# Kernel tuning notes

Hardware: AMD Instinct MI355X
Metric: run time of the kernel (lower is better)

The kernel has to match this reference:

```python
import jax, jax.numpy as jnp
import numpy as np

B, E, H, N = 16, 1024, 16, 2048
Eh = E // H   # head dim = 64
BH = B * H    # 256


def setup_inputs() -> dict:
    key = jax.random.key(0)
    ks = jax.random.split(key, 12)
    query = jax.random.normal(ks[0], (B, E), jnp.float32)
    key_in = jax.random.normal(ks[1], (B, E), jnp.float32)
    value = jax.random.normal(ks[2], (B, E), jnp.float32)
    # State as it would look in steady state: a_sum ~ O(N) positive,
    # q_mem stores already-scaled queries (small), k/v unit-ish scale.
    a_sum_mem = float(N) * (0.9 + 0.2 * jax.random.uniform(ks[3], (BH, N - 1), jnp.float32))
    av_mem = (0.1 * float(N)) * jax.random.normal(ks[4], (BH, N - 1, Eh), jnp.float32)
    q_mem = 0.06 * jax.random.normal(ks[5], (BH, N, Eh), jnp.float32)
    k_t_mem = 0.5 * jax.random.normal(ks[6], (BH, Eh, N), jnp.float32)
    v_mem = 0.5 * jax.random.normal(ks[7], (BH, N, Eh), jnp.float32)
    in_proj_weight = 0.02 * jax.random.normal(ks[8], (3 * E, E), jnp.float32)
    in_proj_bias = jnp.zeros((3 * E,), jnp.float32)
    out_proj_weight = 0.02 * jax.random.normal(ks[9], (E, E), jnp.float32)
    out_proj_bias = jnp.zeros((E,), jnp.float32)
    return dict(query=query, key=key_in, value=value,
                a_sum_mem=a_sum_mem, av_mem=av_mem, q_mem=q_mem,
                k_t_mem=k_t_mem, v_mem=v_mem,
                in_proj_weight=in_proj_weight, in_proj_bias=in_proj_bias,
                out_proj_weight=out_proj_weight, out_proj_bias=out_proj_bias)


def _sdpa_step(a_sum_mem, av_mem, q_mem, k_t_mem, v_mem, q_step, k_step, v_step):
    # Faithful port of _scaled_dot_product_attention_step.
    q_step = q_step / jnp.sqrt(jnp.float32(Eh))          # (BH, Eh)
    q_old = q_mem[:, 0]                                   # (BH, Eh)
    k_old = k_t_mem[:, :, 0]                              # (BH, Eh)
    q_sel = jnp.stack((q_old, q_step), axis=1)            # (BH, 2, Eh)
    k_sel = jnp.stack((k_old, k_step), axis=2)            # (BH, Eh, 2)
    a_tb = jnp.exp(jnp.einsum('bte,bes->bts', q_sel, k_t_mem[:, :, 1:]))  # (BH, 2, N-1)
    a_lr = jnp.exp(jnp.einsum('bne,bet->bnt', q_mem[:, 1:, :], k_sel))    # (BH, N-1, 2)
    a_br = jnp.exp(jnp.sum(q_step * k_step, axis=1))      # (BH,)
    a_sum = jnp.concatenate(
        [a_sum_mem + a_lr[:, :, 1] - a_lr[:, :, 0],
         (a_tb[:, 1].sum(axis=1) + a_br)[:, None]], axis=1)               # (BH, N)
    av_top = (av_mem
              - a_lr[:, :, 0, None] * v_mem[:, 0][:, None, :]
              + a_lr[:, :, 1, None] * v_step[:, None, :])                 # (BH, N-1, Eh)
    av_bot = jnp.einsum('bs,bse->be', a_tb[:, 1], v_mem[:, 1:]) + a_br[:, None] * v_step
    av = jnp.concatenate([av_top, av_bot[:, None, :]], axis=1)            # (BH, N, Eh)
    out = av / a_sum[..., None]
    new_state = (a_sum[:, 1:], av[:, 1:],
                 jnp.concatenate([q_mem[:, 1:], q_step[:, None, :]], axis=1),
                 jnp.concatenate([k_t_mem[:, :, 1:], k_step[:, :, None]], axis=2),
                 jnp.concatenate([v_mem[:, 1:], v_step[:, None, :]], axis=1))
    return out, new_state


def reference(query, key, value, a_sum_mem, av_mem, q_mem, k_t_mem, v_mem,
              in_proj_weight, in_proj_bias, out_proj_weight, out_proj_bias):
    # Packed in-projection (q/k/v chunks of the packed weight).
    w_q, w_k, w_v = jnp.split(in_proj_weight, 3, axis=0)
    b_q, b_k, b_v = jnp.split(in_proj_bias, 3)
    q = (query @ w_q.T + b_q).reshape(BH, Eh)   # head split: (B, H*Eh) -> (B*H, Eh)
    k = (key @ w_k.T + b_k).reshape(BH, Eh)
    v = (value @ w_v.T + b_v).reshape(BH, Eh)
    attn, new_state = _sdpa_step(a_sum_mem, av_mem, q_mem, k_t_mem, v_mem, q, k, v)
    # (BH, N, Eh) -> (N, BH, Eh) -> (N, B, E), then output projection.
    attn = attn.transpose(1, 0, 2).reshape(N, B, E)
    out = attn @ out_proj_weight.T + out_proj_bias    # (N, B, E)
    return (out,) + new_state
```

## Files before the change

kernel.cpp:

```cpp
#include <hip/hip_runtime.h>
#include <hip/hip_bf16.h>

constexpr int kB  = 16;
constexpr int kE  = 1024;
constexpr int kH  = 16;
constexpr int kN  = 2048;
constexpr int kEh = 64;
constexpr int kBH = 256;
constexpr int kM  = kN * kB;

typedef __bf16 bf16x8 __attribute__((ext_vector_type(8)));
typedef float  f32x4  __attribute__((ext_vector_type(4)));
typedef unsigned short u16x4 __attribute__((ext_vector_type(4)));

static __device__ __forceinline__ unsigned short bf16_bits(float f) {
  union { __hip_bfloat16 h; unsigned short u; } cv;
  cv.h = __float2bfloat16(f);
  return cv.u;
}

static __device__ __forceinline__ f32x4 nt_load4(const float* p) {
  return __builtin_nontemporal_load(reinterpret_cast<const f32x4*>(p));
}
static __device__ __forceinline__ void nt_store4(float* p, f32x4 v) {
  __builtin_nontemporal_store(v, reinterpret_cast<f32x4*>(p));
}

__global__ __launch_bounds__(256) void prep_kernel(
    const float* __restrict__ query, const float* __restrict__ key_in,
    const float* __restrict__ value, const float* __restrict__ W,
    const float* __restrict__ bias,
    float* __restrict__ q_step, float* __restrict__ k_step,
    float* __restrict__ v_step,
    const float* __restrict__ wo, __hip_bfloat16* __restrict__ wo_bf) {
  __shared__ float red[4][16];
  int bid = blockIdx.x;
  int tid = threadIdx.x;
  if (bid >= 3072) {
    int i4 = ((bid - 3072) * 256 + tid) * 4;
    f32x4 w4 = nt_load4(wo + i4);
    u16x4 o;
    o[0] = bf16_bits(w4[0]); o[1] = bf16_bits(w4[1]);
    o[2] = bf16_bits(w4[2]); o[3] = bf16_bits(w4[3]);
    *reinterpret_cast<u16x4*>(reinterpret_cast<unsigned short*>(wo_bf) + i4) = o;
    return;
  }
  int j   = bid;
  int mat = j >> 10;
  int col = j & 1023;
  const float* in = (mat == 0) ? query : ((mat == 1) ? key_in : value);
  const float* wrow = W + (size_t)j * kE;

  float4 w4 = reinterpret_cast<const float4*>(wrow)[tid];
  float part[16];
#pragma unroll
  for (int r = 0; r < 16; ++r) {
    float4 in4 = reinterpret_cast<const float4*>(in + (size_t)r * kE)[tid];
    part[r] = w4.x * in4.x + w4.y * in4.y + w4.z * in4.z + w4.w * in4.w;
  }
#pragma unroll
  for (int r = 0; r < 16; ++r) {
    float v = part[r];
    for (int off = 32; off > 0; off >>= 1) v += __shfl_down(v, off, 64);
    part[r] = v;
  }
  int wave = tid >> 6;
  int lane = tid & 63;
  if (lane == 0) {
#pragma unroll
    for (int r = 0; r < 16; ++r) red[wave][r] = part[r];
  }
  __syncthreads();
  if (tid < 16) {
    int r = tid;
    float v = red[0][r] + red[1][r] + red[2][r] + red[3][r] + bias[j];
    int h = col >> 6, eh = col & 63;
    int bh = r * kH + h;
    if (mat == 0)      q_step[bh * kEh + eh] = v * 0.125f;
    else if (mat == 1) k_step[bh * kEh + eh] = v;
    else               v_step[bh * kEh + eh] = v;
  }
}

__global__ __launch_bounds__(256) void stream_kernel(
    const float* __restrict__ q_mem, const float* __restrict__ av_mem,
    const float* __restrict__ a_sum_mem, const float* __restrict__ k_t_mem,
    const float* __restrict__ v_mem, const float* __restrict__ q_step,
    const float* __restrict__ k_step, const float* __restrict__ v_step,
    float* __restrict__ q_out, float* __restrict__ av_out,
    float* __restrict__ a_sum_out, float* __restrict__ k_t_out,
    float* __restrict__ v_out, float* __restrict__ top_sum,
    float* __restrict__ av_last, __hip_bfloat16* __restrict__ attn) {
  __shared__ float qs[64];
  __shared__ float tbuf[1024];
  __shared__ f32x4 redv[4][16];
  __shared__ float redt[4];

  int bid = blockIdx.x;
  int tid = threadIdx.x;
  int wave = tid >> 6, lane = tid & 63;

  if (bid < 8192) {
    int b = bid >> 5;
    int chunk = bid & 31;
    int g = lane >> 4, c = lane & 15;
    int b_ = b >> 4, h = b & 15;

    f32x4 kst  = *reinterpret_cast<const f32x4*>(k_step + (size_t)b * kEh + c * 4);
    f32x4 vst  = *reinterpret_cast<const f32x4*>(v_step + (size_t)b * kEh + c * 4);
    f32x4 vold = *reinterpret_cast<const f32x4*>(v_mem + (size_t)b * kN * kEh + c * 4);
    const float* kt0 = k_t_mem + (size_t)b * kEh * kN;
    f32x4 kold;
    kold[0] = kt0[(size_t)(4 * c + 0) * kN];
    kold[1] = kt0[(size_t)(4 * c + 1) * kN];
    kold[2] = kt0[(size_t)(4 * c + 2) * kN];
    kold[3] = kt0[(size_t)(4 * c + 3) * kN];

    unsigned short* attn_u = reinterpret_cast<unsigned short*>(attn);

    int jb = chunk * 64 + wave * 16;
#pragma unroll
    for (int it = 0; it < 4; ++it) {
      int j = jb + it * 4 + g;
      bool valid = (j <= kN - 2);
      int jc = valid ? j : (kN - 2);

      f32x4 q4 = nt_load4(q_mem + ((size_t)b * kN + (jc + 1)) * kEh + c * 4);
      float p0 = q4[0] * kold[0] + q4[1] * kold[1] + q4[2] * kold[2] + q4[3] * kold[3];
      float p1 = q4[0] * kst[0]  + q4[1] * kst[1]  + q4[2] * kst[2]  + q4[3] * kst[3];
#pragma unroll
      for (int off = 1; off < 16; off <<= 1) {
        p0 += __shfl_xor(p0, off, 64);
        p1 += __shfl_xor(p1, off, 64);
      }
      float a0 = __expf(p0);
      float a1 = __expf(p1);
      float asum = a_sum_mem[(size_t)b * (kN - 1) + jc] + a1 - a0;
      f32x4 av4 = nt_load4(av_mem + ((size_t)b * (kN - 1) + jc) * kEh + c * 4);
      f32x4 avv;
      avv[0] = av4[0] - a0 * vold[0] + a1 * vst[0];
      avv[1] = av4[1] - a0 * vold[1] + a1 * vst[1];
      avv[2] = av4[2] - a0 * vold[2] + a1 * vst[2];
      avv[3] = av4[3] - a0 * vold[3] + a1 * vst[3];

      if (valid) {
        nt_store4(q_out + ((size_t)b * kN + jc) * kEh + c * 4, q4);
        float inv = 1.0f / asum;
        u16x4 pk;
        pk[0] = bf16_bits(avv[0] * inv);
        pk[1] = bf16_bits(avv[1] * inv);
        pk[2] = bf16_bits(avv[2] * inv);
        pk[3] = bf16_bits(avv[3] * inv);
        *reinterpret_cast<u16x4*>(
            attn_u + ((size_t)jc * kB + b_) * kE + h * kEh + c * 4) = pk;
        if (j >= 1) {
          nt_store4(av_out + ((size_t)b * (kN - 1) + (jc - 1)) * kEh + c * 4, avv);
          if (c == 0) a_sum_out[(size_t)b * (kN - 1) + (jc - 1)] = asum;
        }
      }
    }
    return;
  }

  int id2 = bid - 8192;
  int b = id2 >> 1, chunk = id2 & 1;

  if (tid < 64) qs[tid] = q_step[b * kEh + tid];
  __syncthreads();

  int c4 = chunk * 1024 + tid * 4;
  bool last = (c4 + 4 >= kN);
  const float* src = k_t_mem + (size_t)b * kEh * kN;
  float* dst = k_t_out + (size_t)b * kEh * kN;

  f32x4 dot = {0.f, 0.f, 0.f, 0.f};
#pragma unroll 4
  for (int e = 0; e < 64; ++e) {
    f32x4 a = nt_load4(src + (size_t)e * kN + c4);
    float s3 = last ? 0.f
                    : __builtin_nontemporal_load(src + (size_t)e * kN + c4 + 4);
    f32x4 sh;
    sh[0] = a[1]; sh[1] = a[2]; sh[2] = a[3]; sh[3] = s3;
    nt_store4(dst + (size_t)e * kN + c4, sh);
    float q = qs[e];
    dot[0] += q * sh[0];
    dot[1] += q * sh[1];
    dot[2] += q * sh[2];
    dot[3] += q * sh[3];
  }
  float tx = __expf(dot[0]);
  float ty = __expf(dot[1]);
  float tz = __expf(dot[2]);
  float tw = last ? 0.f : __expf(dot[3]);

  tbuf[tid * 4 + 0] = tx;
  tbuf[tid * 4 + 1] = ty;
  tbuf[tid * 4 + 2] = tz;
  tbuf[tid * 4 + 3] = tw;

  float s = tx + ty + tz + tw;
  for (int off = 32; off > 0; off >>= 1) s += __shfl_xor(s, off, 64);
  if (lane == 0) redt[wave] = s;
  __syncthreads();
  if (tid == 0)
    atomicAdd(&top_sum[b], redt[0] + redt[1] + redt[2] + redt[3]);

  int g = lane >> 4, c = lane & 15;
  const float* vsrc = v_mem + (size_t)b * kN * kEh;
  float* vdst = v_out + (size_t)b * kN * kEh;

  f32x4 acc = {0.f, 0.f, 0.f, 0.f};
  int sbase = chunk * 1024 + wave * 256;
#pragma unroll 4
  for (int it = 0; it < 64; ++it) {
    int s4 = sbase + it * 4 + g;
    bool valid = (s4 <= kN - 2);
    int sc = valid ? s4 : (kN - 2);
    float t = valid ? tbuf[s4 - chunk * 1024] : 0.f;
    f32x4 vv = nt_load4(vsrc + (size_t)(sc + 1) * kEh + c * 4);
    acc[0] += t * vv[0];
    acc[1] += t * vv[1];
    acc[2] += t * vv[2];
    acc[3] += t * vv[3];
    if (valid) nt_store4(vdst + (size_t)sc * kEh + c * 4, vv);
  }
#pragma unroll
  for (int off = 16; off <= 32; off <<= 1) {
    acc[0] += __shfl_xor(acc[0], off, 64);
    acc[1] += __shfl_xor(acc[1], off, 64);
    acc[2] += __shfl_xor(acc[2], off, 64);
    acc[3] += __shfl_xor(acc[3], off, 64);
  }
  if (g == 0) redv[wave][c] = acc;
  __syncthreads();
  if (tid < 16) {
    f32x4 a0 = redv[0][tid];
    f32x4 a1 = redv[1][tid];
    f32x4 a2 = redv[2][tid];
    f32x4 a3 = redv[3][tid];
    float* dstl = av_last + (size_t)b * kEh + tid * 4;
    atomicAdd(dstl + 0, a0[0] + a1[0] + a2[0] + a3[0]);
    atomicAdd(dstl + 1, a0[1] + a1[1] + a2[1] + a3[1]);
    atomicAdd(dstl + 2, a0[2] + a1[2] + a2[2] + a3[2]);
    atomicAdd(dstl + 3, a0[3] + a1[3] + a2[3] + a3[3]);
  }
}

__global__ __launch_bounds__(64) void final_kernel(
    const float* __restrict__ q_step, const float* __restrict__ k_step,
    const float* __restrict__ v_step, const float* __restrict__ top_sum,
    const float* __restrict__ av_last_in, float* __restrict__ q_out,
    float* __restrict__ k_t_out, float* __restrict__ v_out,
    float* __restrict__ a_sum_out, float* __restrict__ av_out,
    __hip_bfloat16* __restrict__ attn) {
  int b = blockIdx.x;
  int lane = threadIdx.x;
  int b_ = b >> 4, h = b & 15;
  float qs = q_step[b * kEh + lane];
  float ks = k_step[b * kEh + lane];
  float vs = v_step[b * kEh + lane];
  float p = qs * ks;
  for (int off = 32; off > 0; off >>= 1) p += __shfl_xor(p, off, 64);
  float abr = __expf(p);
  float asum = top_sum[b] + abr;
  float avl = av_last_in[b * kEh + lane] + abr * vs;
  attn[((size_t)(kN - 1) * kB + b_) * kE + h * kEh + lane] =
      __float2bfloat16(avl / asum);
  if (lane == 0) a_sum_out[(size_t)b * (kN - 1) + (kN - 2)] = asum;
  av_out[((size_t)b * (kN - 1) + (kN - 2)) * kEh + lane] = avl;
  q_out[((size_t)b * kN + (kN - 1)) * kEh + lane] = qs;
  k_t_out[(size_t)b * kEh * kN + (size_t)lane * kN + (kN - 1)] = ks;
  v_out[((size_t)b * kN + (kN - 1)) * kEh + lane] = vs;
}

#define BM 128
#define BN 128
#define BK 64

__global__ __launch_bounds__(256) void gemm_kernel(
    const __bf16* __restrict__ A, const __bf16* __restrict__ Bw,
    const float* __restrict__ bias, float* __restrict__ C,
    int M, int Ncols, int K) {
  __shared__ __bf16 lA[BM * BK];
  __shared__ __bf16 lB[BN * BK];
  int tid = threadIdx.x;
  int m0 = blockIdx.x * BM;
  int n0 = blockIdx.y * BN;
  int wave = tid >> 6;
  int lane = tid & 63;
  int wm = (wave & 1) * 64;
  int wn = (wave >> 1) * 64;

  f32x4 zero = {0.f, 0.f, 0.f, 0.f};
  f32x4 acc[4][4];
#pragma unroll
  for (int i = 0; i < 4; ++i)
#pragma unroll
    for (int j = 0; j < 4; ++j) acc[i][j] = zero;

  int quad = lane >> 4;
  int mrow = lane & 15;

  for (int k0 = 0; k0 < K; k0 += BK) {
#pragma unroll
    for (int r = 0; r < 4; ++r) {
      int off = r * 4096 + tid * 16;
      int row = off >> 7;
      int col8 = (off >> 4) & 7;
      const __bf16* ga = A + ((size_t)(m0 + row) * K + k0 + col8 * 8);
      const __bf16* gb = Bw + ((size_t)(n0 + row) * K + k0 + col8 * 8);
      __builtin_amdgcn_global_load_lds(
          (const __attribute__((address_space(1))) void*)ga,
          (__attribute__((address_space(3))) void*)((char*)lA + off), 16, 0, 0);
      __builtin_amdgcn_global_load_lds(
          (const __attribute__((address_space(1))) void*)gb,
          (__attribute__((address_space(3))) void*)((char*)lB + off), 16, 0, 0);
    }
    __syncthreads();

#pragma unroll
    for (int kk = 0; kk < 2; ++kk) {
      bf16x8 af[4], bfr[4];
#pragma unroll
      for (int i = 0; i < 4; ++i) {
        af[i]  = *(const bf16x8*)(&lA[(wm + i * 16 + mrow) * BK + kk * 32 + quad * 8]);
        bfr[i] = *(const bf16x8*)(&lB[(wn + i * 16 + mrow) * BK + kk * 32 + quad * 8]);
      }
#pragma unroll
      for (int i = 0; i < 4; ++i)
#pragma unroll
        for (int j = 0; j < 4; ++j)
          acc[i][j] = __builtin_amdgcn_mfma_f32_16x16x32_bf16(
              af[i], bfr[j], acc[i][j], 0, 0, 0);
    }
    __syncthreads();
  }

  int colq = lane & 15;
  int rowq = lane >> 4;
#pragma unroll
  for (int i = 0; i < 4; ++i) {
#pragma unroll
    for (int j = 0; j < 4; ++j) {
      int col = n0 + wn + j * 16 + colq;
      float bv = bias[col];
      size_t base = (size_t)(m0 + wm + i * 16 + rowq * 4) * Ncols + col;
#pragma unroll
      for (int r = 0; r < 4; ++r) {
        __builtin_nontemporal_store(acc[i][j][r] + bv,
                                    &C[base + (size_t)r * Ncols]);
      }
    }
  }
}

extern "C" void kernel_launch(void* const* d_in, const int* in_sizes, int n_in,
                              void* d_out, int out_size, void* d_ws,
                              size_t ws_size, hipStream_t stream) {
  const float* query          = (const float*)d_in[0];
  const float* key_in         = (const float*)d_in[1];
  const float* value          = (const float*)d_in[2];
  const float* a_sum_mem      = (const float*)d_in[3];
  const float* av_mem         = (const float*)d_in[4];
  const float* q_mem          = (const float*)d_in[5];
  const float* k_t_mem        = (const float*)d_in[6];
  const float* v_mem          = (const float*)d_in[7];
  const float* in_proj_weight = (const float*)d_in[8];
  const float* in_proj_bias   = (const float*)d_in[9];
  const float* out_proj_weight= (const float*)d_in[10];
  const float* out_proj_bias  = (const float*)d_in[11];

  float* out       = (float*)d_out;
  float* a_sum_out = out + (size_t)kN * kB * kE;
  float* av_out    = a_sum_out + (size_t)kBH * (kN - 1);
  float* q_out     = av_out + (size_t)kBH * (kN - 1) * kEh;
  float* k_t_out   = q_out + (size_t)kBH * kN * kEh;
  float* v_out     = k_t_out + (size_t)kBH * kEh * kN;

  char* ws = (char*)d_ws;
  float* q_step  = (float*)ws;
  float* k_step  = q_step + 16384;
  float* v_step  = k_step + 16384;
  float* top_sum = v_step + 16384;
  float* av_last = top_sum + 256;
  __hip_bfloat16* wo_bf   = (__hip_bfloat16*)(ws + 2359296);
  __hip_bfloat16* attn_bf = (__hip_bfloat16*)(ws + 4456448);

  hipMemsetAsync(ws + 196608, 0, 66560, stream);

  prep_kernel<<<4096, 256, 0, stream>>>(query, key_in, value, in_proj_weight,
                                        in_proj_bias, q_step, k_step, v_step,
                                        out_proj_weight, wo_bf);
  stream_kernel<<<8704, 256, 0, stream>>>(q_mem, av_mem, a_sum_mem, k_t_mem,
                                          v_mem, q_step, k_step, v_step, q_out,
                                          av_out, a_sum_out, k_t_out, v_out,
                                          top_sum, av_last, attn_bf);
  final_kernel<<<kBH, 64, 0, stream>>>(q_step, k_step, v_step, top_sum,
                                       av_last, q_out, k_t_out, v_out,
                                       a_sum_out, av_out, attn_bf);
  gemm_kernel<<<dim3(kM / BM, kE / BN), 256, 0, stream>>>(
      (const __bf16*)attn_bf, (const __bf16*)wo_bf, out_proj_bias, out, kM, kE,
      kE);
}
```

Measured before the change: 1.138 ms.

## Double-buffer output GEMM with larger 256x256 tiles and swizzled block order

Rewrites the output-projection GEMM to use 256x256 tiles over 512 threads, with each wave computing a 128x64 sub-tile. LDS staging is now double-buffered, so the next K-slice loads asynchronously while the current one is multiplied, using explicit vmcnt waits. A block-index swizzle groups tiles to improve L2 reuse. The cost is 128 KB of LDS and higher register pressure, which together may limit occupancy to one block per CU.

Result: faster. 1.114 ms (-2.1%).

```diff
diff --git a/kernel.cpp b/kernel.cpp
--- a/kernel.cpp
+++ b/kernel.cpp
@@ -273,82 +273,102 @@
   v_out[((size_t)b * kN + (kN - 1)) * kEh + lane] = vs;
 }
 
-#define BM 128
-#define BN 128
-#define BK 64
-
-__global__ __launch_bounds__(256) void gemm_kernel(
+#define GBM 256
+#define GBN 256
+#define GBK 64
+#define GKT (kE / GBK)
+
+__global__ __launch_bounds__(512, 2) void gemm_kernel(
     const __bf16* __restrict__ A, const __bf16* __restrict__ Bw,
-    const float* __restrict__ bias, float* __restrict__ C,
-    int M, int Ncols, int K) {
-  __shared__ __bf16 lA[BM * BK];
-  __shared__ __bf16 lB[BN * BK];
+    const float* __restrict__ bias, float* __restrict__ C) {
+  __shared__ __bf16 lds[2][2][GBM * GBK];
+
   int tid = threadIdx.x;
-  int m0 = blockIdx.x * BM;
-  int n0 = blockIdx.y * BN;
-  int wave = tid >> 6;
+  int wid = tid >> 6;
   int lane = tid & 63;
-  int wm = (wave & 1) * 64;
-  int wn = (wave >> 1) * 64;
-
-  f32x4 zero = {0.f, 0.f, 0.f, 0.f};
-  f32x4 acc[4][4];
-#pragma unroll
-  for (int i = 0; i < 4; ++i)
-#pragma unroll
-    for (int j = 0; j < 4; ++j) acc[i][j] = zero;
+
+  int bid = blockIdx.x;
+  int swz = (bid & 7) * 64 + (bid >> 3);
+  int mt = swz >> 2;
+  int nt = swz & 3;
+  int m0 = mt * GBM;
+  int n0 = nt * GBN;
+
+  int wm = (wid >> 2) * 128;
+  int wn = (wid & 3) * 64;
 
   int quad = lane >> 4;
   int mrow = lane & 15;
 
-  for (int k0 = 0; k0 < K; k0 += BK) {
-#pragma unroll
-    for (int r = 0; r < 4; ++r) {
-      int off = r * 4096 + tid * 16;
-      int row = off >> 7;
-      int col8 = (off >> 4) & 7;
-      const __bf16* ga = A + ((size_t)(m0 + row) * K + k0 + col8 * 8);
-      const __bf16* gb = Bw + ((size_t)(n0 + row) * K + k0 + col8 * 8);
+  f32x4 acc[8][4];
+#pragma unroll
+  for (int i = 0; i < 8; ++i)
+#pragma unroll
+    for (int j = 0; j < 4; ++j) acc[i][j] = (f32x4){0.f, 0.f, 0.f, 0.f};
+
+  int srow = tid >> 3;
+  int scol = (tid & 7) * 8;
+  const __bf16* gA = A + (size_t)(m0 + srow) * kE + scol;
+  const __bf16* gB = Bw + (size_t)(n0 + srow) * kE + scol;
+
+  auto stage = [&](int t) {
+    int buf = t & 1;
+    int k0 = t * GBK;
+#pragma unroll
+    for (int q = 0; q < 4; ++q) {
       __builtin_amdgcn_global_load_lds(
-          (const __attribute__((address_space(1))) void*)ga,
-          (__attribute__((address_space(3))) void*)((char*)lA + off), 16, 0, 0);
+          (const __attribute__((address_space(1))) void*)(gA + (size_t)q * 64 * kE + k0),
+          (__attribute__((address_space(3))) void*)((char*)&lds[buf][0][0] + q * 8192 + tid * 16),
+          16, 0, 0);
       __builtin_amdgcn_global_load_lds(
-          (const __attribute__((address_space(1))) void*)gb,
-          (__attribute__((address_space(3))) void*)((char*)lB + off), 16, 0, 0);
+          (const __attribute__((address_space(1))) void*)(gB + (size_t)q * 64 * kE + k0),
+          (__attribute__((address_space(3))) void*)((char*)&lds[buf][1][0] + q * 8192 + tid * 16),
+          16, 0, 0);
     }
-    __syncthreads();
-
+  };
+
+  stage(0);
+
+  for (int t = 0; t < GKT; ++t) {
+    if (t + 1 < GKT) stage(t + 1);
+    if (t + 1 < GKT) {
+      asm volatile("s_waitcnt vmcnt(8)" ::: "memory");
+    } else {
+      asm volatile("s_waitcnt vmcnt(0)" ::: "memory");
+    }
+    __builtin_amdgcn_s_barrier();
+
+    const __bf16* la = &lds[t & 1][0][0];
+    const __bf16* lb = &lds[t & 1][1][0];
 #pragma unroll
     for (int kk = 0; kk < 2; ++kk) {
-      bf16x8 af[4], bfr[4];
-#pragma unroll
-      for (int i = 0; i < 4; ++i) {
-        af[i]  = *(const bf16x8*)(&lA[(wm + i * 16 + mrow) * BK + kk * 32 + quad * 8]);
-        bfr[i] = *(const bf16x8*)(&lB[(wn + i * 16 + mrow) * BK + kk * 32 + quad * 8]);
+      bf16x8 bfr[4];
+#pragma unroll
+      for (int j = 0; j < 4; ++j)
+        bfr[j] = *(const bf16x8*)(lb + (wn + j * 16 + mrow) * GBK + kk * 32 + quad * 8);
+#pragma unroll
+      for (int i = 0; i < 8; ++i) {
+        bf16x8 af = *(const bf16x8*)(la + (wm + i * 16 + mrow) * GBK + kk * 32 + quad * 8);
+#pragma unroll
+        for (int j = 0; j < 4; ++j)
+          acc[i][j] = __builtin_amdgcn_mfma_f32_16x16x32_bf16(af, bfr[j], acc[i][j], 0, 0, 0);
       }
-#pragma unroll
-      for (int i = 0; i < 4; ++i)
-#pragma unroll
-        for (int j = 0; j < 4; ++j)
-          acc[i][j] = __builtin_amdgcn_mfma_f32_16x16x32_bf16(
-              af[i], bfr[j], acc[i][j], 0, 0, 0);
     }
-    __syncthreads();
+    __builtin_amdgcn_s_barrier();
   }
 
   int colq = lane & 15;
-  int rowq = lane >> 4;
-#pragma unroll
-  for (int i = 0; i < 4; ++i) {
+  int rowq = (lane >> 4) * 4;
+#pragma unroll
+  for (int i = 0; i < 8; ++i) {
 #pragma unroll
     for (int j = 0; j < 4; ++j) {
       int col = n0 + wn + j * 16 + colq;
       float bv = bias[col];
-      size_t base = (size_t)(m0 + wm + i * 16 + rowq * 4) * Ncols + col;
+      size_t base = (size_t)(m0 + wm + i * 16 + rowq) * kE + col;
 #pragma unroll
       for (int r = 0; r < 4; ++r) {
-        __builtin_nontemporal_store(acc[i][j][r] + bv,
-                                    &C[base + (size_t)r * Ncols]);
+        __builtin_nontemporal_store(acc[i][j][r] + bv, &C[base + (size_t)r * kE]);
       }
     }
   }
@@ -398,7 +418,6 @@
   final_kernel<<<kBH, 64, 0, stream>>>(q_step, k_step, v_step, top_sum,
                                        av_last, q_out, k_t_out, v_out,
                                        a_sum_out, av_out, attn_bf);
-  gemm_kernel<<<dim3(kM / BM, kE / BN), 256, 0, stream>>>(
-      (const __bf16*)attn_bf, (const __bf16*)wo_bf, out_proj_bias, out, kM, kE,
-      kE);
-}
+  gemm_kernel<<<(kM / GBM) * (kE / GBN), 512, 0, stream>>>(
+      (const __bf16*)attn_bf, (const __bf16*)wo_bf, out_proj_bias, out);
+}
```
